# Optimization experiments

Hardware: AMD Instinct MI355X
Metric: run time of the kernel (lower is better)

The kernel has to match this reference:

```python
import jax, jax.numpy as jnp
import numpy as np
import math

SLIDING_WINDOW = 1024  # matches init kwarg

def setup_inputs() -> dict:
    key = jax.random.key(0)
    ks = jax.random.split(key, 6)
    B, S, Hq, Hkv, D = 1, 2048, 32, 8, 128
    NUM_PAGES, STRIDE = 300, 16
    q = jax.random.normal(ks[0], (B, S, Hq, D), dtype=jnp.float32)
    k = jax.random.normal(ks[1], (B, S, Hkv, D), dtype=jnp.float32)
    v = jax.random.normal(ks[2], (B, S, Hkv, D), dtype=jnp.float32)
    sink = jax.random.normal(ks[3], (Hq,), dtype=jnp.float32)
    cache_state = jnp.zeros((NUM_PAGES, STRIDE, 2, Hkv, D), dtype=jnp.float32)
    seq_block_ids = jax.random.randint(ks[4], (B, S // STRIDE), 0, NUM_PAGES, dtype=jnp.int64)
    return {"q": q, "k": k, "v": v, "sink": sink,
            "cache_state": cache_state, "seq_block_ids": seq_block_ids}


def reference(q, k, v, sink, cache_state, seq_block_ids):
    B, S, Hq, D = q.shape
    Hkv = k.shape[2]
    stride = cache_state.shape[1]

    # --- paged cache write (prefill side effect) ---
    kv = jnp.stack([k, v], axis=2)                       # [B,S,2,Hkv,D]
    pages = kv.reshape(B * (S // stride), stride, 2, Hkv, D)
    _ = cache_state.at[seq_block_ids.reshape(-1)].set(pages)

    # --- decomposed attention: matmul + mask + softmax(+sink) + matmul ---
    rep = Hq // Hkv
    ke = jnp.repeat(k, rep, axis=2)                      # [B,S,Hq,D] (GQA expand)
    ve = jnp.repeat(v, rep, axis=2)
    scale = 1.0 / math.sqrt(D)
    scores = jnp.einsum('bihd,bjhd->bhij', q, ke) * scale  # [B,Hq,S,S]

    i = jnp.arange(S)[:, None]
    j = jnp.arange(S)[None, :]
    allowed = (j <= i) & (i - j < SLIDING_WINDOW)        # causal + sliding window
    neg = jnp.finfo(scores.dtype).min
    logits = jnp.where(allowed, scores, neg)

    # attention sink: extra per-head logit appended; contributes to denominator only
    sink_l = jnp.broadcast_to(sink[None, :, None, None], (B, Hq, S, 1))
    probs = jax.nn.softmax(jnp.concatenate([logits, sink_l], axis=-1), axis=-1)[..., :S]

    out = jnp.einsum('bhij,bjhd->bihd', probs, ve)       # [B,S,Hq,D]
    return out
```

## Files before the change

### kernel.cpp

```cpp
#include <hip/hip_runtime.h>
#include <hip/hip_bf16.h>


#define S_LEN 2048
#define DH    128
#define HQ    32
#define HKV   8
#define WIN   1024
#define BR    64
#define BC    32
#define NT    (S_LEN / BC)
#define FM    16.0f
#define TILE_CH 512

typedef unsigned short u16;
typedef __attribute__((ext_vector_type(8))) short  short8;
typedef __attribute__((ext_vector_type(4))) float  floatx4;
typedef __attribute__((ext_vector_type(4))) unsigned int uintx4;

__device__ __forceinline__ unsigned rne1(float a) {
    unsigned u = __float_as_uint(a);
    return (u + 0x7FFFu + ((u >> 16) & 1u)) >> 16;
}
__device__ __forceinline__ unsigned rne_pk(float a, float b) {
    return rne1(a) | (rne1(b) << 16);
}
__device__ __forceinline__ unsigned cvt_pk(float a, float b) {
    unsigned r;
    asm("v_cvt_pk_bf16_f32 %0, %1, %2" : "=v"(r) : "v"(a), "v"(b));
    return r;
}

__global__ __launch_bounds__(256) void pack_kv(const float* __restrict__ kg,
                                               const float* __restrict__ vg,
                                               u16* __restrict__ kp,
                                               u16* __restrict__ vtp)
{
    __shared__ float Vs[BC][DH + 1];
    const int b   = blockIdx.x;
    const int hk  = b >> 6;
    const int jt  = b & 63;
    const int tid = threadIdx.x;
    const int j0  = jt * BC;

    #pragma unroll
    for (int t = 0; t < 4; t++) {
        int idx = tid + t * 256;
        int j   = idx >> 5;
        int dc  = idx & 31;
        floatx4 f = *(const floatx4*)(vg + ((size_t)(j0 + j) * HKV + hk) * DH + dc * 4);
        Vs[j][dc * 4 + 0] = f[0]; Vs[j][dc * 4 + 1] = f[1];
        Vs[j][dc * 4 + 2] = f[2]; Vs[j][dc * 4 + 3] = f[3];
    }

    u16* kpt = kp + (size_t)b * TILE_CH * 8;
    #pragma unroll
    for (int t = 0; t < 2; t++) {
        int c = tid + t * 256;
        int row = c >> 4, cc = c & 15;
        const float* p = kg + ((size_t)(j0 + row) * HKV + hk) * DH + cc * 8;
        floatx4 f0 = *(const floatx4*)p;
        floatx4 f1 = *(const floatx4*)(p + 4);
        int pc = (((row >> 4) * 4 + (cc >> 2)) << 6) | ((cc & 3) << 4) | (row & 15);
        *(uintx4*)(kpt + pc * 8) =
            (uintx4){rne_pk(f0[0], f0[1]), rne_pk(f0[2], f0[3]),
                     rne_pk(f1[0], f1[1]), rne_pk(f1[2], f1[3])};
    }
    __syncthreads();

    u16* vpt = vtp + (size_t)b * TILE_CH * 8;
    #pragma unroll
    for (int t = 0; t < 2; t++) {
        int q  = tid + t * 256;
        int dd = q >> 2, c = q & 3;
        unsigned w0 = rne_pk(Vs[c * 4 + 0][dd], Vs[c * 4 + 16][dd]);
        unsigned w1 = rne_pk(Vs[c * 4 + 1][dd], Vs[c * 4 + 17][dd]);
        unsigned w2 = rne_pk(Vs[c * 4 + 2][dd], Vs[c * 4 + 18][dd]);
        unsigned w3 = rne_pk(Vs[c * 4 + 3][dd], Vs[c * 4 + 19][dd]);
        int qp = ((dd >> 4) << 6) | (c << 4) | (dd & 15);
        *(uintx4*)(vpt + qp * 8) = (uintx4){w0, w1, w2, w3};
    }
}

__launch_bounds__(256, 4)
__global__ void fa_kernel(const float* __restrict__ qg,
                          const u16* __restrict__ kp,
                          const u16* __restrict__ vtp,
                          const float* __restrict__ sg,
                          float* __restrict__ outg)
{
    __shared__ __align__(16) u16 Kt[2][TILE_CH * 8];
    __shared__ __align__(16) u16 Vt[2][TILE_CH * 8];

    const int tid  = threadIdx.x;
    const int w    = tid >> 6;
    const int lane = tid & 63;
    const int quad = lane >> 4;
    const int l16  = lane & 15;

    const int bid  = blockIdx.x;
    const int hk   = bid & 7;
    const int idx  = bid >> 3;
    const int hrem = idx & 3;
    const int u5   = (idx >> 2) & 7;
    const int t4   = idx >> 5;
    const int qbt[4] = {u5, 15 - u5, 16 + u5, 31 - u5};
    const int qb   = qbt[t4];
    const int h    = hk * 4 + hrem;

    {
        const int slot = bid >> 8;
        for (int s = 0; s < slot; s++)
            __builtin_amdgcn_s_sleep(6);
    }

    const int i0 = qb * BR;
    const int m0 = i0 + w * 16;

    short8 qf[4];
    {
        const float* qrow = qg + ((size_t)(m0 + l16) * HQ + h) * DH;
        #pragma unroll
        for (int kk = 0; kk < 4; kk++) {
            const float* p = qrow + kk * 32 + quad * 8;
            floatx4 f0 = *(const floatx4*)p;
            floatx4 f1 = *(const floatx4*)(p + 4);
            uintx4 uq = (uintx4){cvt_pk(f0[0], f0[1]), cvt_pk(f0[2], f0[3]),
                                 cvt_pk(f1[0], f1[1]), cvt_pk(f1[2], f1[3])};
            qf[kk] = *(short8*)&uq;
        }
    }

    short8 ones;
    {
        uintx4 uo = (uintx4){0x3F803F80u, 0x3F803F80u, 0x3F803F80u, 0x3F803F80u};
        ones = *(short8*)&uo;
    }

    const int lane8 = lane * 8;

    floatx4 acc[8];
    #pragma unroll
    for (int i = 0; i < 8; i++) acc[i] = (floatx4){0.f, 0.f, 0.f, 0.f};
    floatx4 acc_l = (floatx4){0.f, 0.f, 0.f, 0.f};

    const int ci  = m0 + l16;
    const int qb4 = quad * 4;

    int jlo = i0 - (WIN - 1); if (jlo < 0) jlo = 0;
    const int jt_lo = jlo >> 5;
    const int jt_hi = (i0 + BR - 1) >> 5;

    const float SC2 = 0.08838834764831845f * 1.4426950408889634f;

    const int ch0 = w * 64 + lane;
    auto stage = [&](int bb, int jt) {
        const u16* kpt = kp  + ((size_t)(hk * NT + jt)) * TILE_CH * 8;
        const u16* vpt = vtp + ((size_t)(hk * NT + jt)) * TILE_CH * 8;
        #pragma unroll
        for (int it = 0; it < 2; it++) {
            int ch = ch0 + it * 256;
            __builtin_amdgcn_global_load_lds(
                (const __attribute__((address_space(1))) unsigned*)(kpt + ch * 8),
                (__attribute__((address_space(3))) unsigned*)(&Kt[bb][ch * 8]), 16, 0, 0);
            __builtin_amdgcn_global_load_lds(
                (const __attribute__((address_space(1))) unsigned*)(vpt + ch * 8),
                (__attribute__((address_space(3))) unsigned*)(&Vt[bb][ch * 8]), 16, 0, 0);
        }
    };

    stage(0, jt_lo);
    int bb = 0;

    for (int jt = jt_lo; jt <= jt_hi; jt++) {
        const int j0 = jt << 5;

        __syncthreads();

        if (jt < jt_hi) stage(bb ^ 1, jt + 1);

        floatx4 ss[2];
        ss[0] = (floatx4){0.f, 0.f, 0.f, 0.f};
        ss[1] = (floatx4){0.f, 0.f, 0.f, 0.f};
        __builtin_amdgcn_s_setprio(1);
        #pragma unroll
        for (int kk = 0; kk < 4; kk++) {
            short8 kf0 = *(const short8*)(&Kt[bb][(kk << 9) + lane8]);
            short8 kf1 = *(const short8*)(&Kt[bb][((4 + kk) << 9) + lane8]);
            ss[0] = __builtin_amdgcn_mfma_f32_16x16x32_bf16(kf0, qf[kk], ss[0], 0, 0, 0);
            ss[1] = __builtin_amdgcn_mfma_f32_16x16x32_bf16(kf1, qf[kk], ss[1], 0, 0, 0);
        }
        __builtin_amdgcn_s_setprio(0);

        short8 vf[8];
        #pragma unroll
        for (int nf = 0; nf < 8; nf++)
            vf[nf] = *(const short8*)(&Vt[bb][(nf << 9) + lane8]);

        float p[2][4];
        const bool interior = (j0 + (BC - 1) <= i0) && (j0 >= i0 + BR - WIN);
        if (interior) {
            #pragma unroll
            for (int n = 0; n < 2; n++)
                #pragma unroll
                for (int r = 0; r < 4; r++)
                    p[n][r] = exp2f(fmaf(ss[n][r], SC2, -FM));
        } else {
            const int dj = ci - j0;
            #pragma unroll
            for (int n = 0; n < 2; n++)
                #pragma unroll
                for (int r = 0; r < 4; r++) {
                    int t = n * 16 + qb4 + r;
                    bool a = (t <= dj) && (t > dj - WIN);
                    p[n][r] = a ? exp2f(fmaf(ss[n][r], SC2, -FM)) : 0.f;
                }
        }

        uintx4 upf = (uintx4){cvt_pk(p[0][0], p[1][0]), cvt_pk(p[0][1], p[1][1]),
                              cvt_pk(p[0][2], p[1][2]), cvt_pk(p[0][3], p[1][3])};
        short8 pf = *(short8*)&upf;

        __builtin_amdgcn_s_setprio(1);
        acc_l = __builtin_amdgcn_mfma_f32_16x16x32_bf16(pf, ones, acc_l, 0, 0, 0);
        #pragma unroll
        for (int nf = 0; nf < 8; nf++) {
            acc[nf] = __builtin_amdgcn_mfma_f32_16x16x32_bf16(pf, vf[nf], acc[nf], 0, 0, 0);
        }
        __builtin_amdgcn_s_setprio(0);
        bb ^= 1;
    }

    const float sk2 = exp2f(fmaf(sg[h], 1.4426950408889634f, -FM));
    float inv_r[4];
    #pragma unroll
    for (int r = 0; r < 4; r++)
        inv_r[r] = 1.f / (acc_l[r] + sk2);
    #pragma unroll
    for (int nf = 0; nf < 8; nf++) {
        int d = nf * 16 + l16;
        #pragma unroll
        for (int r = 0; r < 4; r++) {
            int ig = m0 + qb4 + r;
            outg[((size_t)ig * HQ + h) * DH + d] = acc[nf][r] * inv_r[r];
        }
    }
}

__launch_bounds__(256, 4)
__global__ void fa_fallback(const float* __restrict__ qg,
                            const float* __restrict__ kg,
                            const float* __restrict__ vg,
                            const float* __restrict__ sg,
                            float* __restrict__ outg)
{
    __shared__ __align__(16) u16 Kt[BC * DH];
    __shared__ __align__(16) u16 Vt[DH * BC];
    __shared__ __align__(16) u16 Pb[BR * 40];

    const int tid  = threadIdx.x;
    const int w    = tid >> 6;
    const int lane = tid & 63;
    const int quad = lane >> 4;
    const int l16  = lane & 15;

    const int qb = blockIdx.x / HQ;
    const int h  = blockIdx.x % HQ;
    const int hk = h >> 2;
    const int i0 = qb * BR;
    const int m0 = i0 + w * 16;

    short8 qf[4];
    {
        const float* qrow = qg + ((size_t)(m0 + l16) * HQ + h) * DH;
        #pragma unroll
        for (int kk = 0; kk < 4; kk++) {
            const float* p = qrow + kk * 32 + quad * 8;
            floatx4 f0 = *(const floatx4*)p;
            floatx4 f1 = *(const floatx4*)(p + 4);
            uintx4 u = (uintx4){rne_pk(f0[0], f0[1]), rne_pk(f0[2], f0[3]),
                                rne_pk(f1[0], f1[1]), rne_pk(f1[2], f1[3])};
            qf[kk] = *(short8*)&u;
        }
    }

    floatx4 acc[8];
    #pragma unroll
    for (int i = 0; i < 8; i++) acc[i] = (floatx4){0.f, 0.f, 0.f, 0.f};
    float l_part[4] = {0.f, 0.f, 0.f, 0.f};

    int jlo = i0 - (WIN - 1); if (jlo < 0) jlo = 0;
    const int jt_lo = jlo >> 5;
    const int jt_hi = (i0 + BR - 1) >> 5;
    const float SC2 = 0.08838834764831845f * 1.4426950408889634f;

    for (int jt = jt_lo; jt <= jt_hi; jt++) {
        const int j0 = jt << 5;
        __syncthreads();
        #pragma unroll
        for (int it = 0; it < 2; it++) {
            int g   = tid + 256 * it;
            int row = g >> 4, cc = g & 15;
            int pc  = (row << 4) | (cc ^ (row & 7));
            const float* kpp = kg + ((size_t)(j0 + row) * HKV + hk) * DH + cc * 8;
            floatx4 f0 = *(const floatx4*)kpp;
            floatx4 f1 = *(const floatx4*)(kpp + 4);
            *(uintx4*)(&Kt[pc * 8]) =
                (uintx4){rne_pk(f0[0], f0[1]), rne_pk(f0[2], f0[3]),
                         rne_pk(f1[0], f1[1]), rne_pk(f1[2], f1[3])};
        }
        #pragma unroll
        for (int it = 0; it < 2; it++) {
            int g  = tid + 256 * it;
            int d  = g & 127, jc = g >> 7;
            const float* vp = vg + ((size_t)(j0 + jc * 8) * HKV + hk) * DH + d;
            float e0 = vp[0 * HKV * DH], e1 = vp[1 * HKV * DH];
            float e2 = vp[2 * HKV * DH], e3 = vp[3 * HKV * DH];
            float e4 = vp[4 * HKV * DH], e5 = vp[5 * HKV * DH];
            float e6 = vp[6 * HKV * DH], e7 = vp[7 * HKV * DH];
            int pc = (d << 2) | (jc ^ ((d >> 2) & 3));
            *(uintx4*)(&Vt[pc * 8]) =
                (uintx4){rne_pk(e0, e1), rne_pk(e2, e3), rne_pk(e4, e5), rne_pk(e6, e7)};
        }
        __syncthreads();

        floatx4 sc[2];
        sc[0] = (floatx4){0.f, 0.f, 0.f, 0.f};
        sc[1] = (floatx4){0.f, 0.f, 0.f, 0.f};
        #pragma unroll
        for (int kk = 0; kk < 4; kk++) {
            #pragma unroll
            for (int n = 0; n < 2; n++) {
                int row = n * 16 + l16;
                int cc  = kk * 4 + quad;
                int pc  = (row << 4) | (cc ^ (row & 7));
                short8 kf = *(const short8*)(&Kt[pc * 8]);
                sc[n] = __builtin_amdgcn_mfma_f32_16x16x32_bf16(qf[kk], kf, sc[n], 0, 0, 0);
            }
        }
        #pragma unroll
        for (int r = 0; r < 4; r++) {
            int   i_g = m0 + quad * 4 + r;
            int   jg0 = j0 + l16, jg1 = j0 + 16 + l16;
            bool  a0  = (jg0 <= i_g) && (i_g - jg0 < WIN);
            bool  a1  = (jg1 <= i_g) && (i_g - jg1 < WIN);
            float p0  = a0 ? exp2f(fmaf(sc[0][r], SC2, -FM)) : 0.f;
            float p1  = a1 ? exp2f(fmaf(sc[1][r], SC2, -FM)) : 0.f;
            l_part[r] += p0 + p1;
            int prow = w * 16 + quad * 4 + r;
            *(unsigned*)(&Pb[prow * 40 + 2 * l16]) = rne_pk(p0, p1);
        }
        {
            short8 pf = *(const short8*)(&Pb[(w * 16 + l16) * 40 + quad * 8]);
            #pragma unroll
            for (int nf = 0; nf < 8; nf++) {
                int dd = nf * 16 + l16;
                int qp = (dd << 2) | (quad ^ ((dd >> 2) & 3));
                short8 vf = *(const short8*)(&Vt[qp * 8]);
                acc[nf] = __builtin_amdgcn_mfma_f32_16x16x32_bf16(pf, vf, acc[nf], 0, 0, 0);
            }
        }
    }

    const float sk2 = exp2f(fmaf(sg[h], 1.4426950408889634f, -FM));
    float inv[4];
    #pragma unroll
    for (int r = 0; r < 4; r++) {
        float l = l_part[r];
        #pragma unroll
        for (int off = 1; off < 16; off <<= 1)
            l += __shfl_xor(l, off);
        inv[r] = 1.f / (l + sk2);
    }
    #pragma unroll
    for (int nf = 0; nf < 8; nf++) {
        int d = nf * 16 + l16;
        #pragma unroll
        for (int r = 0; r < 4; r++) {
            int ig = m0 + quad * 4 + r;
            outg[((size_t)ig * HQ + h) * DH + d] = acc[nf][r] * inv[r];
        }
    }
}

extern "C" void kernel_launch(void* const* d_in, const int* in_sizes, int n_in,
                              void* d_out, int out_size, void* d_ws, size_t ws_size,
                              hipStream_t stream) {
    const float* q  = (const float*)d_in[0];
    const float* k  = (const float*)d_in[1];
    const float* v  = (const float*)d_in[2];
    const float* sk = (const float*)d_in[3];
    float* out = (float*)d_out;

    const size_t tile_elems = (size_t)HKV * NT * TILE_CH * 8;
    const size_t need = 2 * tile_elems * sizeof(u16);

    if (ws_size >= need) {
        u16* kp  = (u16*)d_ws;
        u16* vtp = kp + tile_elems;
        pack_kv<<<dim3(HKV * NT), 256, 0, stream>>>(k, v, kp, vtp);
        fa_kernel<<<dim3((S_LEN / BR) * HQ), 256, 0, stream>>>(q, kp, vtp, sk, out);
    } else {
        fa_fallback<<<dim3((S_LEN / BR) * HQ), 256, 0, stream>>>(q, k, v, sk, out);
    }
}
```

Measured before the change: 155.0 us.

## Triple-buffer K tiles and split K/V staging with explicit vmcnt waits

Splits the per-tile K and V async global-to-LDS loads. K now uses a three-deep LDS ring, so it is prefetched two tiles ahead, while V stays double-buffered one tile ahead. The __syncthreads is replaced by an explicit s_waitcnt vmcnt plus s_barrier, so each iteration waits only for the loads it needs and not for all outstanding ones. The aim is more load/compute overlap. The cost is extra LDS, which may reduce occupancy, and a fragile hand-counted vmcnt that must match the number of outstanding loads.

```diff
diff --git a/kernel.cpp b/kernel.cpp
--- a/kernel.cpp
+++ b/kernel.cpp
@@ -89,7 +89,7 @@
                           const float* __restrict__ sg,
                           float* __restrict__ outg)
 {
-    __shared__ __align__(16) u16 Kt[2][TILE_CH * 8];
+    __shared__ __align__(16) u16 Kt[3][TILE_CH * 8];
     __shared__ __align__(16) u16 Vt[2][TILE_CH * 8];
 
     const int tid  = threadIdx.x;
@@ -150,34 +150,47 @@
     int jlo = i0 - (WIN - 1); if (jlo < 0) jlo = 0;
     const int jt_lo = jlo >> 5;
     const int jt_hi = (i0 + BR - 1) >> 5;
+    const int nt    = jt_hi - jt_lo + 1;
 
     const float SC2 = 0.08838834764831845f * 1.4426950408889634f;
 
     const int ch0 = w * 64 + lane;
-    auto stage = [&](int bb, int jt) {
-        const u16* kpt = kp  + ((size_t)(hk * NT + jt)) * TILE_CH * 8;
-        const u16* vpt = vtp + ((size_t)(hk * NT + jt)) * TILE_CH * 8;
+    auto stageK = [&](int b, int jt) {
+        const u16* kpt = kp + ((size_t)(hk * NT + jt)) * TILE_CH * 8;
         #pragma unroll
         for (int it = 0; it < 2; it++) {
             int ch = ch0 + it * 256;
             __builtin_amdgcn_global_load_lds(
                 (const __attribute__((address_space(1))) unsigned*)(kpt + ch * 8),
-                (__attribute__((address_space(3))) unsigned*)(&Kt[bb][ch * 8]), 16, 0, 0);
+                (__attribute__((address_space(3))) unsigned*)(&Kt[b][ch * 8]), 16, 0, 0);
+        }
+    };
+    auto stageV = [&](int b, int jt) {
+        const u16* vpt = vtp + ((size_t)(hk * NT + jt)) * TILE_CH * 8;
+        #pragma unroll
+        for (int it = 0; it < 2; it++) {
+            int ch = ch0 + it * 256;
             __builtin_amdgcn_global_load_lds(
                 (const __attribute__((address_space(1))) unsigned*)(vpt + ch * 8),
-                (__attribute__((address_space(3))) unsigned*)(&Vt[bb][ch * 8]), 16, 0, 0);
+                (__attribute__((address_space(3))) unsigned*)(&Vt[b][ch * 8]), 16, 0, 0);
         }
     };
 
-    stage(0, jt_lo);
-    int bb = 0;
-
-    for (int jt = jt_lo; jt <= jt_hi; jt++) {
-        const int j0 = jt << 5;
-
-        __syncthreads();
-
-        if (jt < jt_hi) stage(bb ^ 1, jt + 1);
+    stageK(0, jt_lo);
+    stageV(0, jt_lo);
+    if (nt > 1) stageK(1, jt_lo + 1);
+
+    int kb = 0, vb = 0;
+    for (int s = 0; s < nt; s++) {
+        if (s + 1 < nt) asm volatile("s_waitcnt vmcnt(2)" ::: "memory");
+        else            asm volatile("s_waitcnt vmcnt(0)" ::: "memory");
+        __builtin_amdgcn_s_barrier();
+        __builtin_amdgcn_sched_barrier(0);
+
+        if (s + 1 < nt) stageV(vb ^ 1, jt_lo + s + 1);
+        if (s + 2 < nt) stageK(kb == 0 ? 2 : kb - 1, jt_lo + s + 2);
+
+        const int j0 = (jt_lo + s) << 5;
 
         floatx4 ss[2];
         ss[0] = (floatx4){0.f, 0.f, 0.f, 0.f};
@@ -185,8 +198,8 @@
         __builtin_amdgcn_s_setprio(1);
         #pragma unroll
         for (int kk = 0; kk < 4; kk++) {
-            short8 kf0 = *(const short8*)(&Kt[bb][(kk << 9) + lane8]);
-            short8 kf1 = *(const short8*)(&Kt[bb][((4 + kk) << 9) + lane8]);
+            short8 kf0 = *(const short8*)(&Kt[kb][(kk << 9) + lane8]);
+            short8 kf1 = *(const short8*)(&Kt[kb][((4 + kk) << 9) + lane8]);
             ss[0] = __builtin_amdgcn_mfma_f32_16x16x32_bf16(kf0, qf[kk], ss[0], 0, 0, 0);
             ss[1] = __builtin_amdgcn_mfma_f32_16x16x32_bf16(kf1, qf[kk], ss[1], 0, 0, 0);
         }
@@ -195,7 +208,7 @@
         short8 vf[8];
         #pragma unroll
         for (int nf = 0; nf < 8; nf++)
-            vf[nf] = *(const short8*)(&Vt[bb][(nf << 9) + lane8]);
+            vf[nf] = *(const short8*)(&Vt[vb][(nf << 9) + lane8]);
 
         float p[2][4];
         const bool interior = (j0 + (BC - 1) <= i0) && (j0 >= i0 + BR - WIN);
@@ -228,7 +241,9 @@
             acc[nf] = __builtin_amdgcn_mfma_f32_16x16x32_bf16(pf, vf[nf], acc[nf], 0, 0, 0);
         }
         __builtin_amdgcn_s_setprio(0);
-        bb ^= 1;
+
+        kb = (kb == 2) ? 0 : kb + 1;
+        vb ^= 1;
     }
 
     const float sk2 = exp2f(fmaf(sg[h], 1.4426950408889634f, -FM));
```

Result: no change. 156.3 us (+0.9%).
